# Performance work log

Measured on AMD Instinct MI355X. Metric: run time of the kernel, lower is better.

Reference implementation:

```python
import jax, jax.numpy as jnp
import numpy as np

B, S, D = 16, 512, 512
H, HS, HSEL = 8, 2, 2      # heads, shared heads, selected routed heads
NB = 2                     # num_block -> L = 3*NB layers (NB knowledge + 2*NB question)
L = 3 * NB
DFF = 2048


def setup_inputs() -> dict:
    key = jax.random.key(0)
    ks = jax.random.split(key, 12)
    s = 0.02
    return {
        'question_emb': jax.random.normal(ks[0], (B, S, D), jnp.float32),
        'interaction_emb': jax.random.normal(ks[1], (B, S, D), jnp.float32),
        'wq': jax.random.normal(ks[2], (L, D, D), jnp.float32) * s,
        'bq': jnp.zeros((L, D), jnp.float32),
        'wv': jax.random.normal(ks[3], (L, D, D), jnp.float32) * s,
        'bv': jnp.zeros((L, D), jnp.float32),
        'wo': jax.random.normal(ks[4], (L, D, D), jnp.float32) * s,
        'bo': jnp.zeros((L, D), jnp.float32),
        'wg': jax.random.normal(ks[5], (L, D, H - HS), jnp.float32) * s,
        'ln1_g': jnp.ones((L, D), jnp.float32),
        'ln1_b': jnp.zeros((L, D), jnp.float32),
        'fw1': jax.random.normal(ks[6], (L, D, DFF), jnp.float32) * s,
        'fb1': jnp.zeros((L, DFF), jnp.float32),
        'fw2': jax.random.normal(ks[7], (L, DFF, D), jnp.float32) * s,
        'fb2': jnp.zeros((L, D), jnp.float32),
        'ln2_g': jnp.ones((L, D), jnp.float32),
        'ln2_b': jnp.zeros((L, D), jnp.float32),
    }


def _ln(x, g, b, eps=1e-5):
    mu = x.mean(-1, keepdims=True)
    var = ((x - mu) ** 2).mean(-1, keepdims=True)
    return g * (x - mu) / jnp.sqrt(var + eps) + b


def _forward(question_emb, interaction_emb, wq, bq, wv, bv, wo, bo, wg,
             ln1_g, ln1_b, fw1, fb1, fw2, fb2, ln2_g, ln2_b):
    def block(x_q, x_v, i, mask_flag, apply_pos):
        b, s, d = x_q.shape
        dk = d // H
        # mask_flag=True -> allow j<=i (strict future masked); False -> allow j<i
        allowed = jnp.tril(jnp.ones((s, s), bool), 0 if mask_flag else -1)
        qlin = x_q @ wq[i] + bq[i]                                   # kq_same: k = q
        v = (x_v @ wv[i] + bv[i]).reshape(b, s, H, dk).transpose(0, 2, 1, 3)
        qh = qlin.reshape(b, s, H, dk).transpose(0, 2, 1, 3)         # [b,h,s,dk]
        scores = jnp.einsum('bhqd,bhkd->bhqk', qh, qh) / jnp.sqrt(jnp.float32(dk))
        scores = jnp.where(allowed[None, None], scores, jnp.float32(-1e9))
        scores = scores.at[:, :, 0, :].set(0.0)                      # pad_zero row 0
        # dynamic head routing over non-shared heads
        gates = jax.nn.softmax((qlin @ wg[i]).reshape(b * s, H - HS), axis=-1)
        _, idx = jax.lax.top_k(gates, HSEL)
        dmask = jnp.zeros_like(gates).at[jnp.arange(b * s)[:, None], idx].set(1.0)
        dyn = (gates * dmask).reshape(b, s, H - HS)
        rmask = jnp.concatenate([jnp.ones((b, s, HS), gates.dtype), dyn], axis=-1)
        rmask = rmask.mean(axis=1)                                   # [b,H]
        attn = jax.nn.softmax(scores, axis=-1)
        ctx = jnp.einsum('bhqk,bhkd->bhqd', attn, v) * rmask[:, :, None, None]
        ctx = ctx.transpose(0, 2, 1, 3).reshape(b, s, d)
        x = _ln(x_q + ctx @ wo[i] + bo[i], ln1_g[i], ln1_b[i])
        if apply_pos:
            ffn = jax.nn.relu(x @ fw1[i] + fb1[i]) @ fw2[i] + fb2[i]
            x = _ln(x + ffn, ln2_g[i], ln2_b[i])
        return x

    y = interaction_emb
    for i in range(NB):                 # knowledge encoder
        y = block(y, y, i, True, False)
    x = question_emb
    li = NB
    for j in range(2 * NB):             # question encoder, alternating
        if j % 2 == 0:
            x = block(x, x, li, True, False)
        else:
            x = block(x, y, li, False, True)
        li += 1
    return x


def reference(question_emb, interaction_emb, wq, bq, wv, bv, wo, bo, wg,
              ln1_g, ln1_b, fw1, fb1, fw2, fb2, ln2_g, ln2_b):
    return _forward(question_emb, interaction_emb, wq, bq, wv, bv, wo, bo, wg,
                    ln1_g, ln1_b, fw1, fb1, fw2, fb2, ln2_g, ln2_b)
```

## Files before the change

### kernel.cpp

```cpp
#include <hip/hip_runtime.h>
#include <hip/hip_bf16.h>

#define BSZ 16
#define SEQ 512
#define DIM 512
#define NH 8
#define DK 64
#define NROWS (BSZ*SEQ)
#define DFF2 2048

typedef unsigned short u16;
typedef u16   u16x8 __attribute__((ext_vector_type(8)));
typedef short s16x8 __attribute__((ext_vector_type(8)));
typedef float f32x4 __attribute__((ext_vector_type(4)));

__device__ __forceinline__ u16 f2b(float x) {
    union { float f; unsigned int u; } c; c.f = x;
    unsigned int r = c.u + 0x7fff + ((c.u >> 16) & 1);
    return (u16)(r >> 16);
}
__device__ __forceinline__ float b2f(u16 u) {
    union { unsigned int i; float f; } c; c.i = ((unsigned int)u) << 16; return c.f;
}

__device__ __forceinline__ void gld16(const u16* g, u16* l) {
    __builtin_amdgcn_global_load_lds(
        (const __attribute__((address_space(1))) unsigned int*)(unsigned long long)g,
        (__attribute__((address_space(3))) unsigned int*)(unsigned int)(unsigned long long)l,
        16, 0, 0);
}

__global__ __launch_bounds__(256) void cast_dual(const float* __restrict__ in,
                                                 float* __restrict__ fcopy,
                                                 u16* __restrict__ out, int n4) {
    int i = blockIdx.x * 256 + threadIdx.x;
    if (i >= n4) return;
    float4 v = ((const float4*)in)[i];
    ((float4*)fcopy)[i] = v;
    ushort4 o; o.x = f2b(v.x); o.y = f2b(v.y); o.z = f2b(v.z); o.w = f2b(v.w);
    ((ushort4*)out)[i] = o;
}

__global__ __launch_bounds__(256) void transpose_cast(
    const float* __restrict__ W, u16* __restrict__ WT,
    int K, int N, int layer0, int lstride, size_t dstride)
{
    __shared__ float t[32][33];
    int z = blockIdx.z;
    const float* Wz = W + (size_t)(layer0 + z * lstride) * K * N;
    u16* WTz = WT + (size_t)z * dstride;
    int k0 = blockIdx.x * 32, n0 = blockIdx.y * 32;
    int tx = threadIdx.x & 31, ty = threadIdx.x >> 5;
    for (int i = ty; i < 32; i += 8) t[i][tx] = Wz[(size_t)(k0 + i) * N + n0 + tx];
    __syncthreads();
    for (int i = ty; i < 32; i += 8) WTz[(size_t)(n0 + i) * K + k0 + tx] = f2b(t[tx][i]);
}

template<int WRITE_BF16, int RELU, int SPLIT, int SPLITK, int NI>
__global__ __launch_bounds__(256) void gemm2(
    const u16* __restrict__ Aq, const u16* __restrict__ Av,
    const u16* __restrict__ WT,
    const float* __restrict__ bias1, const float* __restrict__ bias2,
    void* __restrict__ C1, void* __restrict__ C2,
    int K, int lda, int ldw, int ldc, int nsplit, int nx)
{
    __shared__ __attribute__((aligned(16))) u16 smem[2 * 128 * 32 + 2 * NI * 32 * 32];
    u16* As = smem;
    u16* Bs = smem + 2 * 128 * 32;
    int tid = threadIdx.x;
    int wave = tid >> 6, lane = tid & 63;
    int quad = lane >> 4, l16 = lane & 15;

    int bid = blockIdx.x;
    int per = gridDim.x >> 3;
    int swz = (bid & 7) * per + (bid >> 3);
    int nxy = SPLITK ? ((int)gridDim.x >> 1) : (int)gridDim.x;
    int kslice = 0;
    if (SPLITK && swz >= nxy) { kslice = 1; swz -= nxy; }
    int bx = swz % nx, by = swz / nx;
    int n0 = bx * (NI * 32), m0 = by * 128;

    int wrow = (wave & 1) * 64;
    int wcol = (wave >> 1) * (NI * 16);
    bool isv = SPLIT && (n0 >= nsplit);
    const u16* A = isv ? Av : Aq;

    int sr = wave * 32 + (lane >> 2);
    int sc = (lane & 3) * 8;
    int ko = kslice * K;
    const u16* gA0 = A  + (size_t)(m0 + sr) * lda + sc + ko;
    const u16* gA1 = gA0 + (size_t)16 * lda;
    int lo0 = (wave * 32) * 32;
    int lo1 = (wave * 32 + 16) * 32;

    const u16* gB0;
    const u16* gB1 = nullptr;
    int bo0, bo1 = 0;
    if (NI == 4) {
        gB0 = WT + (size_t)(n0 + sr) * ldw + sc + ko;
        gB1 = gB0 + (size_t)16 * ldw;
        bo0 = lo0; bo1 = lo1;
    } else {
        gB0 = WT + (size_t)(n0 + wave * 16 + (lane >> 2)) * ldw + sc + ko;
        bo0 = (wave * 16) * 32;
    }

    f32x4 acc[4][NI];
    #pragma unroll
    for (int i = 0; i < 4; i++)
        #pragma unroll
        for (int j = 0; j < NI; j++) acc[i][j] = (f32x4){0.f, 0.f, 0.f, 0.f};

    gld16(gA0, &As[lo0]);
    gld16(gA1, &As[lo1]);
    gld16(gB0, &Bs[bo0]);
    if (NI == 4) gld16(gB1, &Bs[bo1]);
    __syncthreads();

    int NT = K >> 5;
    int cur = 0;
    for (int t = 0; t < NT; ++t) {
        if (t + 1 < NT) {
            int k0 = (t + 1) << 5;
            int nxt = cur ^ 1;
            gld16(gA0 + k0, &As[nxt * 128 * 32 + lo0]);
            gld16(gA1 + k0, &As[nxt * 128 * 32 + lo1]);
            gld16(gB0 + k0, &Bs[nxt * NI * 32 * 32 + bo0]);
            if (NI == 4) gld16(gB1 + k0, &Bs[nxt * NI * 32 * 32 + bo1]);
        }
        s16x8 af[4], bf[NI];
        #pragma unroll
        for (int i = 0; i < 4; i++)
            af[i] = *(s16x8*)&As[cur * 128 * 32 + (wrow + i * 16 + l16) * 32 + quad * 8];
        #pragma unroll
        for (int i = 0; i < NI; i++)
            bf[i] = *(s16x8*)&Bs[cur * NI * 32 * 32 + (wcol + i * 16 + l16) * 32 + quad * 8];
        #pragma unroll
        for (int mi = 0; mi < 4; mi++)
            #pragma unroll
            for (int ni = 0; ni < NI; ni++)
                acc[mi][ni] = __builtin_amdgcn_mfma_f32_16x16x32_bf16(
                    af[mi], bf[ni], acc[mi][ni], 0, 0, 0);
        __syncthreads();
        cur ^= 1;
    }

    const float* bias = isv ? bias2 : bias1;
    void* C = (isv || (SPLITK && kslice)) ? C2 : C1;
    int nb = n0 - (isv ? nsplit : 0);

    if (WRITE_BF16) {
        const int CSTR = NI * 32 + 8;
        u16* Cs = smem;
        #pragma unroll
        for (int ni = 0; ni < NI; ni++) {
            int lc_ = wcol + ni * 16 + l16;
            float bb = bias ? bias[nb + lc_] : 0.f;
            #pragma unroll
            for (int mi = 0; mi < 4; mi++) {
                int lrow = wrow + mi * 16 + quad * 4;
                #pragma unroll
                for (int r = 0; r < 4; r++) {
                    float v = acc[mi][ni][r] + bb;
                    if (RELU) v = fmaxf(v, 0.f);
                    Cs[(lrow + r) * CSTR + lc_] = f2b(v);
                }
            }
        }
        __syncthreads();
        const int CPR = NI * 4;
        int row = tid / CPR;
        int col = (tid % CPR) * 8;
        #pragma unroll
        for (int i = 0; i < NI * 2; i++) {
            int rr = row + i * (256 / CPR);
            u16x8 vv = *(u16x8*)&Cs[rr * CSTR + col];
            *(u16x8*)((u16*)C + (size_t)(m0 + rr) * ldc + nb + col) = vv;
        }
    } else {
        #pragma unroll
        for (int ni = 0; ni < NI; ni++) {
            int cn = nb + wcol + ni * 16 + l16;
            float bb = bias ? bias[cn] : 0.f;
            #pragma unroll
            for (int mi = 0; mi < 4; mi++) {
                int cm = m0 + wrow + mi * 16 + quad * 4;
                #pragma unroll
                for (int r = 0; r < 4; r++) {
                    size_t off = (size_t)(cm + r) * ldc + cn;
                    float v = acc[mi][ni][r] + bb;
                    if (RELU) v = fmaxf(v, 0.f);
                    ((float*)C)[off] = v;
                }
            }
        }
    }
}

__global__ void init_rmask6(float* __restrict__ r) {
    int t = blockIdx.x * 256 + threadIdx.x;
    if (t < 6 * 128) r[t] = ((t & 7) < 2) ? 1.0f : 0.0f;
}

__global__ __launch_bounds__(256) void router_kernel(
    const u16* __restrict__ qlin, const float* __restrict__ wg,
    float* __restrict__ rmask)
{
    __shared__ float s_wg[6 * 544];
    __shared__ float sacc[8];
    int tid = threadIdx.x;
    #pragma unroll
    for (int k = 0; k < 12; k++) {
        int n = tid + k * 256;
        int d = n / 6, r = n - d * 6;
        s_wg[r * 544 + (d >> 4) * 17 + (d & 15)] = wg[n];
    }
    if (tid < 8) sacc[tid] = 0.f;
    __syncthreads();

    int c = tid & 31;
    int row = blockIdx.x * 8 + (tid >> 5);
    int cb = c * 17;
    const u16* xr = qlin + (size_t)row * DIM + c * 16;
    u16x8 q0 = *(const u16x8*)xr;
    u16x8 q1 = *(const u16x8*)(xr + 8);

    float lg[6] = {0.f, 0.f, 0.f, 0.f, 0.f, 0.f};
    #pragma unroll
    for (int j = 0; j < 8; j++) {
        float x = b2f(q0[j]);
        #pragma unroll
        for (int r = 0; r < 6; r++) lg[r] += x * s_wg[r * 544 + cb + j];
    }
    #pragma unroll
    for (int j = 0; j < 8; j++) {
        float x = b2f(q1[j]);
        #pragma unroll
        for (int r = 0; r < 6; r++) lg[r] += x * s_wg[r * 544 + cb + 8 + j];
    }
    #pragma unroll
    for (int r = 0; r < 6; r++) {
        #pragma unroll
        for (int o = 1; o < 32; o <<= 1) lg[r] += __shfl_xor(lg[r], o);
    }
    float m = lg[0];
    #pragma unroll
    for (int r = 1; r < 6; r++) m = fmaxf(m, lg[r]);
    float s = 0.f;
    #pragma unroll
    for (int r = 0; r < 6; r++) { lg[r] = __expf(lg[r] - m); s += lg[r]; }
    float inv = 1.0f / s;
    #pragma unroll
    for (int r = 0; r < 6; r++) lg[r] *= inv;
    int i1 = 0; float g1 = lg[0];
    #pragma unroll
    for (int r = 1; r < 6; r++) if (lg[r] > g1) { g1 = lg[r]; i1 = r; }
    int i2 = -1; float g2 = -1.f;
    #pragma unroll
    for (int r = 0; r < 6; r++) if (r != i1 && lg[r] > g2) { g2 = lg[r]; i2 = r; }
    if (c == 0) {
        atomicAdd(&sacc[i1], g1);
        atomicAdd(&sacc[i2], g2);
    }
    __syncthreads();
    if (tid < 6) {
        int b = blockIdx.x >> 6;
        atomicAdd(&rmask[b * 8 + 2 + tid], sacc[tid] * (1.0f / (float)SEQ));
    }
}

__global__ __launch_bounds__(256) void transpose_v(
    const u16* __restrict__ v, u16* __restrict__ vT)
{
    __shared__ u16 t[64][72];
    int jt = blockIdx.x, bh = blockIdx.y;
    int b = bh >> 3, h = bh & 7;
    int tid = threadIdx.x;
    int lr = tid >> 2, lc = (tid & 3) * 16;
    const u16* src = v + (size_t)(b * SEQ + jt * 64 + lr) * DIM + h * DK + lc;
    *(u16x8*)&t[lr][lc]     = *(const u16x8*)src;
    *(u16x8*)&t[lr][lc + 8] = *(const u16x8*)(src + 8);
    __syncthreads();
    u16x8 o0, o1;
    #pragma unroll
    for (int i = 0; i < 8; i++) o0[i] = t[lc + i][lr];
    #pragma unroll
    for (int i = 0; i < 8; i++) o1[i] = t[lc + 8 + i][lr];
    u16* dst = vT + ((size_t)bh * DK + lr) * SEQ + jt * 64 + lc;
    *(u16x8*)dst       = o0;
    *(u16x8*)(dst + 8) = o1;
}

__global__ __launch_bounds__(512) void attn_flash(
    const u16* __restrict__ qlin, const u16* __restrict__ vT,
    const float* __restrict__ rmask, u16* __restrict__ ctx, int mask_flag)
{
    __shared__ u16 s_k [64][72];
    __shared__ u16 s_vt[64][72];
    __shared__ u16 s_p [128][72];
    int gi = (blockIdx.x & 7) * ((int)gridDim.x >> 3) + (blockIdx.x >> 3);
    int qt = gi & 3, h = (gi >> 2) & 7, b = gi >> 5;
    int tid = threadIdx.x;
    int wave = tid >> 6, lane = tid & 63;
    int quad = lane >> 4, l16 = lane & 15;
    int lr = tid >> 3, lc = (tid & 7) * 8;

    const u16* qbase = qlin + (size_t)(b * SEQ) * DIM + h * DK;
    const u16* vbase = vT + (size_t)(b * NH + h) * DK * SEQ;

    int qg0 = qt * 128 + wave * 16 + quad * 4;
    s16x8 aq[2];
    #pragma unroll
    for (int ks = 0; ks < 2; ks++)
        aq[ks] = *(const s16x8*)(qbase + (size_t)(qt * 128 + wave * 16 + l16) * DIM
                                 + ks * 32 + quad * 8);

    u16x8 k0 = *(const u16x8*)(qbase + (size_t)lr * DIM + lc);
    u16x8 v0 = *(const u16x8*)(vbase + (size_t)lr * SEQ + lc);

    f32x4 acc_o[4];
    #pragma unroll
    for (int i = 0; i < 4; i++) acc_o[i] = (f32x4){0.f, 0.f, 0.f, 0.f};
    float m_i[4] = {-1e30f, -1e30f, -1e30f, -1e30f};
    float l_i[4] = {0.f, 0.f, 0.f, 0.f};

    int rmax = qt * 128 + wave * 16 + 15;
    int jt_end = 2 * qt + 1;
    for (int jt = 0; jt <= jt_end; jt++) {
        __syncthreads();
        *(u16x8*)&s_k [lr][lc] = k0;
        *(u16x8*)&s_vt[lr][lc] = v0;
        __syncthreads();
        if (jt < jt_end) {
            k0 = *(const u16x8*)(qbase + (size_t)((jt + 1) * 64 + lr) * DIM + lc);
            v0 = *(const u16x8*)(vbase + (size_t)lr * SEQ + (jt + 1) * 64 + lc);
        }

        bool active = (jt * 64) <= (mask_flag ? rmax : rmax - 1);
        if (active) {
            f32x4 acc_s[4];
            #pragma unroll
            for (int i = 0; i < 4; i++) acc_s[i] = (f32x4){0.f, 0.f, 0.f, 0.f};
            #pragma unroll
            for (int ks = 0; ks < 2; ks++) {
                #pragma unroll
                for (int nf = 0; nf < 4; nf++) {
                    s16x8 bb = *(s16x8*)&s_k[nf * 16 + l16][ks * 32 + quad * 8];
                    acc_s[nf] = __builtin_amdgcn_mfma_f32_16x16x32_bf16(aq[ks], bb, acc_s[nf], 0, 0, 0);
                }
            }

            float sc[4][4];
            #pragma unroll
            for (int nf = 0; nf < 4; nf++) {
                int jg = jt * 64 + nf * 16 + l16;
                #pragma unroll
                for (int r = 0; r < 4; r++) {
                    float v = acc_s[nf][r] * 0.125f;
                    int bound = mask_flag ? (qg0 + r) : (qg0 + r - 1);
                    if (jg > bound) v = -1e30f;
                    sc[nf][r] = v;
                }
            }
            float tmax[4];
            #pragma unroll
            for (int r = 0; r < 4; r++) {
                float t = fmaxf(fmaxf(sc[0][r], sc[1][r]), fmaxf(sc[2][r], sc[3][r]));
                #pragma unroll
                for (int o = 1; o < 16; o <<= 1) t = fmaxf(t, __shfl_xor(t, o));
                tmax[r] = t;
            }
            float p[4][4];
            #pragma unroll
            for (int r = 0; r < 4; r++) {
                float mnew = fmaxf(m_i[r], tmax[r]);
                float alpha = __expf(m_i[r] - mnew);
                float su = 0.f;
                #pragma unroll
                for (int nf = 0; nf < 4; nf++) { p[nf][r] = __expf(sc[nf][r] - mnew); su += p[nf][r]; }
                #pragma unroll
                for (int o = 1; o < 16; o <<= 1) su += __shfl_xor(su, o);
                l_i[r] = l_i[r] * alpha + su;
                m_i[r] = mnew;
                #pragma unroll
                for (int nf = 0; nf < 4; nf++) acc_o[nf][r] *= alpha;
            }
            #pragma unroll
            for (int nf = 0; nf < 4; nf++)
                #pragma unroll
                for (int r = 0; r < 4; r++)
                    s_p[wave * 16 + quad * 4 + r][nf * 16 + l16] = f2b(p[nf][r]);
            __builtin_amdgcn_wave_barrier();
            s16x8 pa[2];
            pa[0] = *(s16x8*)&s_p[wave * 16 + l16][quad * 8];
            pa[1] = *(s16x8*)&s_p[wave * 16 + l16][32 + quad * 8];
            __builtin_amdgcn_wave_barrier();

            #pragma unroll
            for (int ks = 0; ks < 2; ks++) {
                #pragma unroll
                for (int nf = 0; nf < 4; nf++) {
                    s16x8 bb = *(s16x8*)&s_vt[nf * 16 + l16][ks * 32 + quad * 8];
                    acc_o[nf] = __builtin_amdgcn_mfma_f32_16x16x32_bf16(pa[ks], bb, acc_o[nf], 0, 0, 0);
                }
            }
        }
    }

    float rm = rmask[b * 8 + h];
    int qrow = qt * 128 + wave * 16 + quad * 4;
    #pragma unroll
    for (int r = 0; r < 4; r++) {
        float scale = rm / l_i[r];
        u16* dst = ctx + (size_t)(b * SEQ + qrow + r) * DIM + h * DK;
        #pragma unroll
        for (int nf = 0; nf < 4; nf++)
            dst[nf * 16 + l16] = f2b(acc_o[nf][r] * scale);
    }
}

__global__ __launch_bounds__(256) void attn_row0(
    const u16* __restrict__ vT, const float* __restrict__ rmask, u16* __restrict__ ctx)
{
    int bh = blockIdx.x;
    int b = bh >> 3, h = bh & 7;
    int d = threadIdx.x >> 2, seg = threadIdx.x & 3;
    const u16* src = vT + ((size_t)bh * DK + d) * SEQ + seg * 128;
    float s = 0.f;
    for (int i = 0; i < 16; i++) {
        u16x8 v = *(const u16x8*)(src + i * 8);
        #pragma unroll
        for (int j = 0; j < 8; j++) s += b2f(v[j]);
    }
    s += __shfl_down(s, 1);
    s += __shfl_down(s, 2);
    if (seg == 0)
        ctx[(size_t)(b * SEQ) * DIM + h * DK + d] =
            f2b(s * (1.0f / (float)SEQ) * rmask[b * 8 + h]);
}

__global__ __launch_bounds__(256) void add_ln2(
    float* __restrict__ x, const u16* __restrict__ p0, const u16* __restrict__ p1,
    const float* __restrict__ bcol,
    const float* __restrict__ g, const float* __restrict__ bta,
    u16* __restrict__ out16)
{
    __shared__ float redA[4], redB[4];
    int row = blockIdx.x, tid = threadIdx.x;
    size_t base = (size_t)row * DIM;
    float t0 = x[base + tid]       + b2f(p0[base + tid])       + b2f(p1[base + tid])       + bcol[tid];
    float t1 = x[base + tid + 256] + b2f(p0[base + tid + 256]) + b2f(p1[base + tid + 256]) + bcol[tid + 256];
    float s = t0 + t1, sq = t0 * t0 + t1 * t1;
    for (int o = 32; o > 0; o >>= 1) { s += __shfl_down(s, o, 64); sq += __shfl_down(sq, o, 64); }
    int lane = tid & 63, wid = tid >> 6;
    if (lane == 0) { redA[wid] = s; redB[wid] = sq; }
    __syncthreads();
    float S1 = redA[0] + redA[1] + redA[2] + redA[3];
    float S2 = redB[0] + redB[1] + redB[2] + redB[3];
    float mu = S1 * (1.0f / (float)DIM);
    float var = S2 * (1.0f / (float)DIM) - mu * mu;
    float rstd = rsqrtf(var + 1e-5f);
    float o0 = g[tid]       * (t0 - mu) * rstd + bta[tid];
    float o1 = g[tid + 256] * (t1 - mu) * rstd + bta[tid + 256];
    x[base + tid]       = o0;
    x[base + tid + 256] = o1;
    out16[base + tid]       = f2b(o0);
    out16[base + tid + 256] = f2b(o1);
}

extern "C" void kernel_launch(void* const* d_in, const int* in_sizes, int n_in,
                              void* d_out, int out_size, void* d_ws, size_t ws_size,
                              hipStream_t stream) {
    const float* qe   = (const float*)d_in[0];
    const float* ie   = (const float*)d_in[1];
    const float* wq   = (const float*)d_in[2];
    const float* bq   = (const float*)d_in[3];
    const float* wv   = (const float*)d_in[4];
    const float* bv   = (const float*)d_in[5];
    const float* wo   = (const float*)d_in[6];
    const float* bo   = (const float*)d_in[7];
    const float* wg   = (const float*)d_in[8];
    const float* ln1g = (const float*)d_in[9];
    const float* ln1b = (const float*)d_in[10];
    const float* fw1  = (const float*)d_in[11];
    const float* fb1  = (const float*)d_in[12];
    const float* fw2  = (const float*)d_in[13];
    const float* fb2  = (const float*)d_in[14];
    const float* ln2g = (const float*)d_in[15];
    const float* ln2b = (const float*)d_in[16];

    const size_t RD = (size_t)NROWS * DIM;
    float* ws   = (float*)d_ws;
    float* xbuf = ws;
    float* ybuf = ws + RD;

    u16* b16    = (u16*)(ws + 2 * RD);
    u16* x16    = b16;                 b16 += RD;
    u16* y16    = b16;                 b16 += RD;
    u16* ctx16  = b16;                 b16 += RD;
    u16* qlin16 = b16;                 b16 += RD;
    u16* vbuf16 = b16;                 b16 += RD;
    u16* vT     = b16;                 b16 += RD;
    u16* proj0  = vbuf16;
    u16* hid    = b16;                 b16 += 4 * RD;
    u16* proj1  = b16;                 b16 += RD;
    u16* wqvT   = b16;                 b16 += 6 * (size_t)1024 * 512;
    u16* woT    = b16;                 b16 += 6 * (size_t)512 * 512;
    u16* fw1T   = b16;                 b16 += 2 * (size_t)DFF2 * 512;
    u16* fw2T   = b16;                 b16 += 2 * (size_t)512 * DFF2;
    float* rmask6 = (float*)b16;

    cast_dual<<<(int)(RD / 4 / 256), 256, 0, stream>>>(qe, xbuf, x16, (int)(RD / 4));
    cast_dual<<<(int)(RD / 4 / 256), 256, 0, stream>>>(ie, ybuf, y16, (int)(RD / 4));

    transpose_cast<<<dim3(16, 16, 6), 256, 0, stream>>>(wq, wqvT,             512, 512, 0, 1, (size_t)1024 * 512);
    transpose_cast<<<dim3(16, 16, 6), 256, 0, stream>>>(wv, wqvT + 512 * 512, 512, 512, 0, 1, (size_t)1024 * 512);
    transpose_cast<<<dim3(16, 16, 6), 256, 0, stream>>>(wo, woT,              512, 512, 0, 1, (size_t)512 * 512);
    transpose_cast<<<dim3(16, 64, 2), 256, 0, stream>>>(fw1, fw1T, 512, DFF2, 3, 2, (size_t)DFF2 * 512);
    transpose_cast<<<dim3(64, 16, 2), 256, 0, stream>>>(fw2, fw2T, DFF2, 512, 3, 2, (size_t)512 * DFF2);
    init_rmask6<<<3, 256, 0, stream>>>(rmask6);

    const int BIG = 1 << 30;
    auto run_block = [&](float* xr, u16* xq16, const u16* xv16, int l, int maskf, int pos) {
        size_t lD = (size_t)l * DIM;
        float* rm = rmask6 + l * 128;
        gemm2<1, 0, 1, 0, 2><<<1024, 256, 0, stream>>>(
            xq16, xv16, wqvT + (size_t)l * 1024 * 512, bq + lD, bv + lD,
            qlin16, vbuf16, 512, 512, 512, 512, 512, 16);
        transpose_v<<<dim3(8, 128), 256, 0, stream>>>(vbuf16, vT);
        router_kernel<<<NROWS / 8, 256, 0, stream>>>(qlin16, wg + (size_t)l * DIM * 6, rm);
        attn_flash<<<512, 512, 0, stream>>>(qlin16, vT, rm, ctx16, maskf);
        attn_row0<<<128, 256, 0, stream>>>(vT, rm, ctx16);
        gemm2<1, 0, 0, 1, 2><<<1024, 256, 0, stream>>>(
            ctx16, ctx16, woT + (size_t)l * 512 * 512, nullptr, nullptr,
            proj0, proj1, 256, 512, 512, 512, BIG, 8);
        add_ln2<<<NROWS, 256, 0, stream>>>(xr, proj0, proj1, bo + lD,
                                           ln1g + lD, ln1b + lD, xq16);
        if (pos) {
            int slot = (l - 3) / 2;
            gemm2<1, 1, 0, 0, 2><<<2048, 256, 0, stream>>>(
                xq16, xq16, fw1T + (size_t)slot * DFF2 * 512,
                fb1 + (size_t)l * DFF2, nullptr,
                hid, nullptr, 512, 512, 512, DFF2, BIG, 32);
            gemm2<1, 0, 0, 1, 2><<<1024, 256, 0, stream>>>(
                hid, hid, fw2T + (size_t)slot * 512 * DFF2, nullptr, nullptr,
                proj0, proj1, 1024, DFF2, DFF2, 512, BIG, 8);
            add_ln2<<<NROWS, 256, 0, stream>>>(xr, proj0, proj1, fb2 + lD,
                                               ln2g + lD, ln2b + lD, xq16);
        }
    };

    run_block(ybuf, y16, y16, 0, 1, 0);
    run_block(ybuf, y16, y16, 1, 1, 0);
    run_block(xbuf, x16, x16, 2, 1, 0);
    run_block(xbuf, x16, y16, 3, 0, 1);
    run_block(xbuf, x16, x16, 4, 1, 0);
    run_block(xbuf, x16, y16, 5, 0, 1);

    const size_t nBytes = RD * sizeof(float);
    hipMemcpyAsync(d_out, xbuf, nBytes, hipMemcpyDeviceToDevice, stream);
}
```

Before: 837.5 us.

## Fuse V transpose into QV GEMM epilogue and write final LN to output

The QV projection GEMM gains a template flag that makes its V half write bf16 results straight into the transposed [b,h,dk,seq] layout. This removes the separate transpose_v kernel and one round trip of the V buffer through memory. The last layer's add+LayerNorm now writes straight into the output buffer, so the trailing device-to-device copy is dropped. The transposed stores are 8-byte writes strided by SEQ, which may coalesce worse than the old tiled transpose.

```diff
diff --git a/kernel.cpp b/kernel.cpp
--- a/kernel.cpp
+++ b/kernel.cpp
@@ -11,6 +11,7 @@
 
 typedef unsigned short u16;
 typedef u16   u16x8 __attribute__((ext_vector_type(8)));
+typedef u16   u16x4 __attribute__((ext_vector_type(4)));
 typedef short s16x8 __attribute__((ext_vector_type(8)));
 typedef float f32x4 __attribute__((ext_vector_type(4)));
 
@@ -56,7 +57,7 @@
     for (int i = ty; i < 32; i += 8) WTz[(size_t)(n0 + i) * K + k0 + tx] = f2b(t[tx][i]);
 }
 
-template<int WRITE_BF16, int RELU, int SPLIT, int SPLITK, int NI>
+template<int WRITE_BF16, int RELU, int SPLIT, int SPLITK, int NI, int VT>
 __global__ __launch_bounds__(256) void gemm2(
     const u16* __restrict__ Aq, const u16* __restrict__ Av,
     const u16* __restrict__ WT,
@@ -145,6 +146,25 @@
         cur ^= 1;
     }
 
+    if (VT && isv) {
+        int bI = m0 >> 9, j0 = m0 & 511;
+        u16* dst = (u16*)C2 + ((size_t)(bI * NH * DK) + (n0 - nsplit)) * SEQ + j0;
+        #pragma unroll
+        for (int ni = 0; ni < NI; ni++) {
+            int lc_ = wcol + ni * 16 + l16;
+            float bb = bias2[(n0 - nsplit) + lc_];
+            #pragma unroll
+            for (int mi = 0; mi < 4; mi++) {
+                int jj = wrow + mi * 16 + quad * 4;
+                u16x4 tv;
+                #pragma unroll
+                for (int r = 0; r < 4; r++) tv[r] = f2b(acc[mi][ni][r] + bb);
+                *(u16x4*)(dst + (size_t)lc_ * SEQ + jj) = tv;
+            }
+        }
+        return;
+    }
+
     const float* bias = isv ? bias2 : bias1;
     void* C = (isv || (SPLITK && kslice)) ? C2 : C1;
     int nb = n0 - (isv ? nsplit : 0);
@@ -267,28 +287,6 @@
         int b = blockIdx.x >> 6;
         atomicAdd(&rmask[b * 8 + 2 + tid], sacc[tid] * (1.0f / (float)SEQ));
     }
-}
-
-__global__ __launch_bounds__(256) void transpose_v(
-    const u16* __restrict__ v, u16* __restrict__ vT)
-{
-    __shared__ u16 t[64][72];
-    int jt = blockIdx.x, bh = blockIdx.y;
-    int b = bh >> 3, h = bh & 7;
-    int tid = threadIdx.x;
-    int lr = tid >> 2, lc = (tid & 3) * 16;
-    const u16* src = v + (size_t)(b * SEQ + jt * 64 + lr) * DIM + h * DK + lc;
-    *(u16x8*)&t[lr][lc]     = *(const u16x8*)src;
-    *(u16x8*)&t[lr][lc + 8] = *(const u16x8*)(src + 8);
-    __syncthreads();
-    u16x8 o0, o1;
-    #pragma unroll
-    for (int i = 0; i < 8; i++) o0[i] = t[lc + i][lr];
-    #pragma unroll
-    for (int i = 0; i < 8; i++) o1[i] = t[lc + 8 + i][lr];
-    u16* dst = vT + ((size_t)bh * DK + lr) * SEQ + jt * 64 + lc;
-    *(u16x8*)dst       = o0;
-    *(u16x8*)(dst + 8) = o1;
 }
 
 __global__ __launch_bounds__(512) void attn_flash(
@@ -440,7 +438,8 @@
 }
 
 __global__ __launch_bounds__(256) void add_ln2(
-    float* __restrict__ x, const u16* __restrict__ p0, const u16* __restrict__ p1,
+    const float* __restrict__ x, float* __restrict__ xout,
+    const u16* __restrict__ p0, const u16* __restrict__ p1,
     const float* __restrict__ bcol,
     const float* __restrict__ g, const float* __restrict__ bta,
     u16* __restrict__ out16)
@@ -462,8 +461,8 @@
     float rstd = rsqrtf(var + 1e-5f);
     float o0 = g[tid]       * (t0 - mu) * rstd + bta[tid];
     float o1 = g[tid + 256] * (t1 - mu) * rstd + bta[tid + 256];
-    x[base + tid]       = o0;
-    x[base + tid + 256] = o1;
+    xout[base + tid]       = o0;
+    xout[base + tid + 256] = o1;
     out16[base + tid]       = f2b(o0);
     out16[base + tid + 256] = f2b(o1);
 }
@@ -499,9 +498,8 @@
     u16* y16    = b16;                 b16 += RD;
     u16* ctx16  = b16;                 b16 += RD;
     u16* qlin16 = b16;                 b16 += RD;
-    u16* vbuf16 = b16;                 b16 += RD;
+    u16* proj0  = b16;                 b16 += RD;
     u16* vT     = b16;                 b16 += RD;
-    u16* proj0  = vbuf16;
     u16* hid    = b16;                 b16 += 4 * RD;
     u16* proj1  = b16;                 b16 += RD;
     u16* wqvT   = b16;                 b16 += 6 * (size_t)1024 * 512;
@@ -521,42 +519,39 @@
     init_rmask6<<<3, 256, 0, stream>>>(rmask6);
 
     const int BIG = 1 << 30;
-    auto run_block = [&](float* xr, u16* xq16, const u16* xv16, int l, int maskf, int pos) {
+    auto run_block = [&](float* xr, u16* xq16, const u16* xv16, int l, int maskf, int pos,
+                         float* xo2) {
         size_t lD = (size_t)l * DIM;
         float* rm = rmask6 + l * 128;
-        gemm2<1, 0, 1, 0, 2><<<1024, 256, 0, stream>>>(
+        gemm2<1, 0, 1, 0, 2, 1><<<1024, 256, 0, stream>>>(
             xq16, xv16, wqvT + (size_t)l * 1024 * 512, bq + lD, bv + lD,
-            qlin16, vbuf16, 512, 512, 512, 512, 512, 16);
-        transpose_v<<<dim3(8, 128), 256, 0, stream>>>(vbuf16, vT);
+            qlin16, vT, 512, 512, 512, 512, 512, 16);
         router_kernel<<<NROWS / 8, 256, 0, stream>>>(qlin16, wg + (size_t)l * DIM * 6, rm);
         attn_flash<<<512, 512, 0, stream>>>(qlin16, vT, rm, ctx16, maskf);
         attn_row0<<<128, 256, 0, stream>>>(vT, rm, ctx16);
-        gemm2<1, 0, 0, 1, 2><<<1024, 256, 0, stream>>>(
+        gemm2<1, 0, 0, 1, 2, 0><<<1024, 256, 0, stream>>>(
             ctx16, ctx16, woT + (size_t)l * 512 * 512, nullptr, nullptr,
             proj0, proj1, 256, 512, 512, 512, BIG, 8);
-        add_ln2<<<NROWS, 256, 0, stream>>>(xr, proj0, proj1, bo + lD,
+        add_ln2<<<NROWS, 256, 0, stream>>>(xr, xr, proj0, proj1, bo + lD,
                                            ln1g + lD, ln1b + lD, xq16);
         if (pos) {
             int slot = (l - 3) / 2;
-            gemm2<1, 1, 0, 0, 2><<<2048, 256, 0, stream>>>(
+            gemm2<1, 1, 0, 0, 2, 0><<<2048, 256, 0, stream>>>(
                 xq16, xq16, fw1T + (size_t)slot * DFF2 * 512,
                 fb1 + (size_t)l * DFF2, nullptr,
                 hid, nullptr, 512, 512, 512, DFF2, BIG, 32);
-            gemm2<1, 0, 0, 1, 2><<<1024, 256, 0, stream>>>(
+            gemm2<1, 0, 0, 1, 2, 0><<<1024, 256, 0, stream>>>(
                 hid, hid, fw2T + (size_t)slot * 512 * DFF2, nullptr, nullptr,
                 proj0, proj1, 1024, DFF2, DFF2, 512, BIG, 8);
-            add_ln2<<<NROWS, 256, 0, stream>>>(xr, proj0, proj1, fb2 + lD,
+            add_ln2<<<NROWS, 256, 0, stream>>>(xr, xo2, proj0, proj1, fb2 + lD,
                                                ln2g + lD, ln2b + lD, xq16);
         }
     };
 
-    run_block(ybuf, y16, y16, 0, 1, 0);
-    run_block(ybuf, y16, y16, 1, 1, 0);
-    run_block(xbuf, x16, x16, 2, 1, 0);
-    run_block(xbuf, x16, y16, 3, 0, 1);
-    run_block(xbuf, x16, x16, 4, 1, 0);
-    run_block(xbuf, x16, y16, 5, 0, 1);
-
-    const size_t nBytes = RD * sizeof(float);
-    hipMemcpyAsync(d_out, xbuf, nBytes, hipMemcpyDeviceToDevice, stream);
-}
+    run_block(ybuf, y16, y16, 0, 1, 0, ybuf);
+    run_block(ybuf, y16, y16, 1, 1, 0, ybuf);
+    run_block(xbuf, x16, x16, 2, 1, 0, xbuf);
+    run_block(xbuf, x16, y16, 3, 0, 1, xbuf);
+    run_block(xbuf, x16, x16, 4, 1, 0, xbuf);
+    run_block(xbuf, x16, y16, 5, 0, 1, (float*)d_out);
+}
```

Measured after the change: 816.1 us. 1.03x faster.
